# Kernel optimization log

Measured on AMD Instinct MI355X. Metric: run time of the kernel, lower is better.

## Reference

```python
import jax, jax.numpy as jnp
import numpy as np

NUM_CLASSES = 1000  # label vocabulary size (matches fill_max for label)
B = 16384
D_IN = 1024   # image_embedding
D_OUT = 256   # projection_dim


def setup_inputs() -> dict:
    key = jax.random.key(0)
    k = jax.random.split(key, 6)
    x = jax.random.normal(k[0], (B, D_IN), dtype=jnp.float32)
    label = jax.random.randint(k[1], (B,), 0, NUM_CLASSES, dtype=jnp.int64)
    scale = 1.0 / np.sqrt(D_IN)
    W1_w = jax.random.normal(k[2], (D_OUT, D_IN), dtype=jnp.float32) * scale
    W1_b = jax.random.normal(k[3], (D_OUT,), dtype=jnp.float32) * scale
    W2_w = jax.random.normal(k[4], (D_OUT, D_IN), dtype=jnp.float32) * scale
    W2_b = jax.random.normal(k[5], (D_OUT,), dtype=jnp.float32) * scale
    return {"x": x, "label": label, "W1_w": W1_w, "W1_b": W1_b,
            "W2_w": W2_w, "W2_b": W2_b}


def reference(x, label, W1_w, W1_b, W2_w, W2_b):
    # Leave-one-group-out mean, vectorized via segment sums.
    # Original: for each i, mean of x[label != label_i] (detached); zeros if none.
    b = x.shape[0]
    xd = jax.lax.stop_gradient(x)  # .detach() in the torch code
    label_sum = jax.ops.segment_sum(xd, label, num_segments=NUM_CLASSES)          # [C, D_IN]
    label_cnt = jax.ops.segment_sum(jnp.ones((b,), dtype=x.dtype), label,
                                    num_segments=NUM_CLASSES)                     # [C]
    total_sum = xd.sum(axis=0)                                                    # [D_IN]
    other_sum = total_sum[None, :] - label_sum[label]                             # [B, D_IN]
    other_cnt = jnp.asarray(b, x.dtype) - label_cnt[label]                        # [B]
    calculate_mean = jnp.where(other_cnt[:, None] > 0,
                               other_sum / jnp.maximum(other_cnt, 1)[:, None],
                               jnp.zeros((), x.dtype))                            # [B, D_IN]
    # W1(x) + W2(calculate_mean)  (torch Linear: y = x @ W.T + b)
    return x @ W1_w.T + W1_b + calculate_mean @ W2_w.T + W2_b
```

## Files before the change

kernel.cpp:

```cpp
#include <hip/hip_runtime.h>
#include <hip/hip_bf16.h>

constexpr int B      = 16384;
constexpr int D_IN   = 1024;
constexpr int D_OUT  = 256;
constexpr int NCLS   = 1000;
constexpr int CPAD   = 1024;

constexpr size_t OFF_XB   = 0;
constexpr size_t OFF_WB   = OFF_XB  + (size_t)B * D_IN * 2;
constexpr size_t OFF_S    = OFF_WB  + (size_t)512 * D_IN * 2;
constexpr size_t OFF_Z    = OFF_S   + (size_t)CPAD * D_IN * 4;
constexpr size_t OFF_T    = OFF_Z   + (size_t)CPAD * D_OUT * 4;
constexpr size_t OFF_CNT  = OFF_T   + (size_t)D_IN * 4;
constexpr size_t OFF_OFFS = OFF_CNT + (size_t)CPAD * 4;
constexpr size_t OFF_CUR  = OFF_OFFS+ (size_t)CPAD * 4;
constexpr size_t OFF_ROWL = OFF_CUR + (size_t)CPAD * 4;

typedef short bf16x8 __attribute__((ext_vector_type(8)));
typedef float f32x4  __attribute__((ext_vector_type(4)));

__device__ __forceinline__ unsigned short f2bf(float f) {
    unsigned int u = __float_as_uint(f);
    return (unsigned short)((u + 0x7FFFu + ((u >> 16) & 1u)) >> 16);
}

__device__ __forceinline__ void cvt8(const float4& a, const float4& b, unsigned short* dst) {
    union { unsigned short u[8]; bf16x8 v; } r;
    r.u[0] = f2bf(a.x); r.u[1] = f2bf(a.y); r.u[2] = f2bf(a.z); r.u[3] = f2bf(a.w);
    r.u[4] = f2bf(b.x); r.u[5] = f2bf(b.y); r.u[6] = f2bf(b.z); r.u[7] = f2bf(b.w);
    *(bf16x8*)dst = r.v;
}

__device__ __forceinline__ ushort4 f2bf4(const float4& a) {
    ushort4 r;
    r.x = f2bf(a.x); r.y = f2bf(a.y); r.z = f2bf(a.z); r.w = f2bf(a.w);
    return r;
}

__device__ __forceinline__ void async16(const unsigned short* g, unsigned short* l) {
    __builtin_amdgcn_global_load_lds(
        (const __attribute__((address_space(1))) void*)g,
        (__attribute__((address_space(3))) void*)l,
        16, 0, 0);
}

__global__ void cvtw_zero_kernel(const float* __restrict__ W1, const float* __restrict__ W2,
                                 unsigned short* __restrict__ Wb,
                                 int* __restrict__ cnt, float* __restrict__ T,
                                 float* __restrict__ Z) {
    int lin = blockIdx.x * blockDim.x + threadIdx.x;
    int i = lin * 8;
    const float* src = (i < D_OUT * D_IN) ? (W1 + i) : (W2 + (i - D_OUT * D_IN));
    float4 a = *(const float4*)(src);
    float4 b = *(const float4*)(src + 4);
    cvt8(a, b, Wb + i);
    if (lin < CPAD) { cnt[lin] = 0; T[lin] = 0.f; }
    *(float4*)(Z + (size_t)lin * 4) = float4{0.f, 0.f, 0.f, 0.f};
}

__global__ void hist_kernel(const int* __restrict__ label, int* __restrict__ cnt) {
    int i = blockIdx.x * blockDim.x + threadIdx.x;
    atomicAdd(&cnt[label[i]], 1);
}

__global__ __launch_bounds__(1024)
void scan_kernel(const int* __restrict__ cnt, int* __restrict__ offs, int* __restrict__ cursor) {
    __shared__ int bufA[1024];
    __shared__ int bufB[1024];
    int t = threadIdx.x;
    int v = cnt[t];
    bufA[t] = v;
    __syncthreads();
    int* src = bufA;
    int* dst = bufB;
    for (int off = 1; off < 1024; off <<= 1) {
        int sv = src[t];
        if (t >= off) sv += src[t - off];
        dst[t] = sv;
        __syncthreads();
        int* tmp = src; src = dst; dst = tmp;
    }
    int excl = src[t] - v;
    offs[t] = excl;
    cursor[t] = excl;
}

__global__ void scatter_kernel(const int* __restrict__ label,
                               int* __restrict__ cursor,
                               int* __restrict__ rowlist) {
    int i = blockIdx.x * blockDim.x + threadIdx.x;
    int c = label[i];
    int p = atomicAdd(&cursor[c], 1);
    rowlist[p] = i;
}

__global__ void segsum_kernel(const float* __restrict__ x,
                              const int* __restrict__ offs,
                              const int* __restrict__ cnt,
                              const int* __restrict__ rowlist,
                              float* __restrict__ s,
                              unsigned short* __restrict__ xb) {
    int c = blockIdx.x;
    int col = threadIdx.x * 4;
    float4 acc = {0.f, 0.f, 0.f, 0.f};
    if (c < NCLS) {
        int o = offs[c], n = cnt[c];
        int r = 0;
        for (; r + 4 <= n; r += 4) {
            int i0 = rowlist[o + r + 0];
            int i1 = rowlist[o + r + 1];
            int i2 = rowlist[o + r + 2];
            int i3 = rowlist[o + r + 3];
            float4 v0 = *(const float4*)(x + (size_t)i0 * D_IN + col);
            float4 v1 = *(const float4*)(x + (size_t)i1 * D_IN + col);
            float4 v2 = *(const float4*)(x + (size_t)i2 * D_IN + col);
            float4 v3 = *(const float4*)(x + (size_t)i3 * D_IN + col);
            *(ushort4*)(xb + (size_t)i0 * D_IN + col) = f2bf4(v0);
            *(ushort4*)(xb + (size_t)i1 * D_IN + col) = f2bf4(v1);
            *(ushort4*)(xb + (size_t)i2 * D_IN + col) = f2bf4(v2);
            *(ushort4*)(xb + (size_t)i3 * D_IN + col) = f2bf4(v3);
            acc.x += (v0.x + v1.x) + (v2.x + v3.x);
            acc.y += (v0.y + v1.y) + (v2.y + v3.y);
            acc.z += (v0.z + v1.z) + (v2.z + v3.z);
            acc.w += (v0.w + v1.w) + (v2.w + v3.w);
        }
        for (; r < n; ++r) {
            int i0 = rowlist[o + r];
            float4 v = *(const float4*)(x + (size_t)i0 * D_IN + col);
            *(ushort4*)(xb + (size_t)i0 * D_IN + col) = f2bf4(v);
            acc.x += v.x; acc.y += v.y; acc.z += v.z; acc.w += v.w;
        }
    }
    *(float4*)(s + (size_t)c * D_IN + col) = acc;
}

__global__ void tsum_kernel(const float* __restrict__ s, float* __restrict__ T) {
    int col = threadIdx.x * 4;
    int c0 = blockIdx.x * 16;
    float4 acc = {0.f, 0.f, 0.f, 0.f};
#pragma unroll 4
    for (int c = 0; c < 16; ++c) {
        float4 v = *(const float4*)(s + (size_t)(c0 + c) * D_IN + col);
        acc.x += v.x; acc.y += v.y; acc.z += v.z; acc.w += v.w;
    }
    atomicAdd(&T[col + 0], acc.x);
    atomicAdd(&T[col + 1], acc.y);
    atomicAdd(&T[col + 2], acc.z);
    atomicAdd(&T[col + 3], acc.w);
}

__global__ __launch_bounds__(256)
void meanz_kernel(const float* __restrict__ s,
                  const float* __restrict__ T,
                  const int* __restrict__ cnt,
                  const unsigned short* __restrict__ Wb,
                  const float* __restrict__ b2,
                  float* __restrict__ Z) {
    __shared__ unsigned short As[64 * 32];
    __shared__ unsigned short Bs[64 * 32];

    const int tid  = threadIdx.x;
    const int wave = tid >> 6;
    const int lane = tid & 63;
    const int quad = lane >> 4;
    const int l16  = lane & 15;
    const int bm   = blockIdx.x * 64;
    const int bn   = blockIdx.y * 64;
    const int kb   = blockIdx.z * 256;
    const int wm   = (wave >> 1) * 32;
    const int wn   = (wave & 1) * 32;

    const int arow = tid >> 2;
    const int akc  = (tid & 3) * 8;

    const int cls = bm + arow;
    const int d   = B - cnt[cls];
    const float scale = (d > 0) ? 1.f / (float)d : 0.f;
    const float* sp = s + (size_t)cls * D_IN + akc;
    const float* tp = T + akc;

    const int bidx = wave * 64 + lane;
    const int brow = bidx >> 2;
    const int bkc  = (bidx & 3) * 8;
    const unsigned short* bp = Wb + (size_t)(256 + bn + brow) * D_IN + bkc;

    f32x4 acc[2][2] = {};

    for (int k0 = kb; k0 < kb + 256; k0 += 32) {
        float4 s0 = *(const float4*)(sp + k0);
        float4 s1 = *(const float4*)(sp + k0 + 4);
        float4 t0 = *(const float4*)(tp + k0);
        float4 t1 = *(const float4*)(tp + k0 + 4);
        __syncthreads();
        async16(bp + k0, Bs + wave * 512);
        float4 m0 = {(t0.x - s0.x) * scale, (t0.y - s0.y) * scale,
                     (t0.z - s0.z) * scale, (t0.w - s0.w) * scale};
        float4 m1 = {(t1.x - s1.x) * scale, (t1.y - s1.y) * scale,
                     (t1.z - s1.z) * scale, (t1.w - s1.w) * scale};
        cvt8(m0, m1, As + arow * 32 + akc);
        __syncthreads();

        bf16x8 af[2], bfr[2];
#pragma unroll
        for (int t = 0; t < 2; ++t) {
            af[t]  = *(const bf16x8*)&As[(wm + t * 16 + l16) * 32 + quad * 8];
            bfr[t] = *(const bf16x8*)&Bs[(wn + t * 16 + l16) * 32 + quad * 8];
        }
#pragma unroll
        for (int i = 0; i < 2; ++i)
#pragma unroll
            for (int j = 0; j < 2; ++j)
                acc[i][j] = __builtin_amdgcn_mfma_f32_16x16x32_bf16(af[i], bfr[j], acc[i][j], 0, 0, 0);
    }

    const bool addb = (blockIdx.z == 0);
#pragma unroll
    for (int j = 0; j < 2; ++j) {
        const int n = bn + wn + j * 16 + l16;
        const float bias = addb ? b2[n] : 0.f;
#pragma unroll
        for (int i = 0; i < 2; ++i)
#pragma unroll
            for (int r = 0; r < 4; ++r) {
                const int c = bm + wm + i * 16 + quad * 4 + r;
                atomicAdd(&Z[(size_t)c * D_OUT + n], acc[i][j][r] + bias);
            }
    }
}

__global__ __launch_bounds__(256)
void gemm1_kernel(const unsigned short* __restrict__ xb,
                  const unsigned short* __restrict__ Wb,
                  const float* __restrict__ b1,
                  const float* __restrict__ Z,
                  const int* __restrict__ label,
                  float* __restrict__ out) {
    __shared__ unsigned short As[64 * 32];
    __shared__ unsigned short Bs[64 * 32];

    const int tid  = threadIdx.x;
    const int wave = tid >> 6;
    const int lane = tid & 63;
    const int quad = lane >> 4;
    const int l16  = lane & 15;
    const int bm   = blockIdx.x * 64;
    const int bn   = blockIdx.y * 64;
    const int wm   = (wave >> 1) * 32;
    const int wn   = (wave & 1) * 32;

    const int idx = wave * 64 + lane;
    const int row = idx >> 2;
    const int kc  = (idx & 3) * 8;
    const unsigned short* ap = xb + (size_t)(bm + row) * D_IN + kc;
    const unsigned short* bp = Wb + (size_t)(bn + row) * D_IN + kc;

    f32x4 acc[2][2] = {};

    for (int k0 = 0; k0 < D_IN; k0 += 32) {
        __syncthreads();
        async16(ap + k0, As + wave * 512);
        async16(bp + k0, Bs + wave * 512);
        __syncthreads();

        bf16x8 af[2], bfr[2];
#pragma unroll
        for (int t = 0; t < 2; ++t) {
            af[t]  = *(const bf16x8*)&As[(wm + t * 16 + l16) * 32 + quad * 8];
            bfr[t] = *(const bf16x8*)&Bs[(wn + t * 16 + l16) * 32 + quad * 8];
        }
#pragma unroll
        for (int i = 0; i < 2; ++i)
#pragma unroll
            for (int j = 0; j < 2; ++j)
                acc[i][j] = __builtin_amdgcn_mfma_f32_16x16x32_bf16(af[i], bfr[j], acc[i][j], 0, 0, 0);
    }

    int zrow[2][4];
#pragma unroll
    for (int i = 0; i < 2; ++i)
#pragma unroll
        for (int r = 0; r < 4; ++r)
            zrow[i][r] = label[bm + wm + i * 16 + quad * 4 + r] * D_OUT;

#pragma unroll
    for (int j = 0; j < 2; ++j) {
        const int n = bn + wn + j * 16 + l16;
        const float bias = b1[n];
#pragma unroll
        for (int i = 0; i < 2; ++i)
#pragma unroll
            for (int r = 0; r < 4; ++r) {
                const int m = bm + wm + i * 16 + quad * 4 + r;
                out[(size_t)m * D_OUT + n] = acc[i][j][r] + bias + Z[zrow[i][r] + n];
            }
    }
}

extern "C" void kernel_launch(void* const* d_in, const int* in_sizes, int n_in,
                              void* d_out, int out_size, void* d_ws, size_t ws_size,
                              hipStream_t stream) {
    const float* x    = (const float*)d_in[0];
    const int*   lab  = (const int*)d_in[1];
    const float* W1_w = (const float*)d_in[2];
    const float* W1_b = (const float*)d_in[3];
    const float* W2_w = (const float*)d_in[4];
    const float* W2_b = (const float*)d_in[5];
    float* out = (float*)d_out;

    char* ws = (char*)d_ws;
    unsigned short* xb = (unsigned short*)(ws + OFF_XB);
    unsigned short* Wb = (unsigned short*)(ws + OFF_WB);
    float* s   = (float*)(ws + OFF_S);
    float* Z   = (float*)(ws + OFF_Z);
    float* T   = (float*)(ws + OFF_T);
    int* cnt     = (int*)(ws + OFF_CNT);
    int* offs    = (int*)(ws + OFF_OFFS);
    int* cursor  = (int*)(ws + OFF_CUR);
    int* rowlist = (int*)(ws + OFF_ROWL);

    cvtw_zero_kernel<<<256, 256, 0, stream>>>(W1_w, W2_w, Wb, cnt, T, Z);
    hist_kernel<<<64, 256, 0, stream>>>(lab, cnt);
    scan_kernel<<<1, 1024, 0, stream>>>(cnt, offs, cursor);
    scatter_kernel<<<64, 256, 0, stream>>>(lab, cursor, rowlist);
    segsum_kernel<<<CPAD, 256, 0, stream>>>(x, offs, cnt, rowlist, s, xb);
    tsum_kernel<<<64, 256, 0, stream>>>(s, T);
    dim3 zgrid(CPAD / 64, D_OUT / 64, 4);
    meanz_kernel<<<zgrid, 256, 0, stream>>>(s, T, cnt, Wb, W2_b, Z);
    dim3 ggrid(B / 64, D_OUT / 64);
    gemm1_kernel<<<ggrid, 256, 0, stream>>>(xb, Wb, W1_b, Z, lab, out);
}
```

Before: 164.6 us.

## Fuse histogram/scan/scatter into per-class segsum scan and double K-step in GEMMs

Removes the separate histogram, scan and scatter launches. Each class block now scans all labels itself to collect its row list in shared memory and writes its own count. Both GEMM kernels now process 64 K elements per barrier pair instead of 32, and gemm1 prefetches bias and Z values before the main loop. This trades three small launches and global atomics for redundant label reads across 1024 blocks. The shared row buffer is capped at 512 rows per class, which the random labels fit but skewed labels could overflow.

```diff
diff --git a/kernel.cpp b/kernel.cpp
--- a/kernel.cpp
+++ b/kernel.cpp
@@ -13,9 +13,6 @@
 constexpr size_t OFF_Z    = OFF_S   + (size_t)CPAD * D_IN * 4;
 constexpr size_t OFF_T    = OFF_Z   + (size_t)CPAD * D_OUT * 4;
 constexpr size_t OFF_CNT  = OFF_T   + (size_t)D_IN * 4;
-constexpr size_t OFF_OFFS = OFF_CNT + (size_t)CPAD * 4;
-constexpr size_t OFF_CUR  = OFF_OFFS+ (size_t)CPAD * 4;
-constexpr size_t OFF_ROWL = OFF_CUR + (size_t)CPAD * 4;
 
 typedef short bf16x8 __attribute__((ext_vector_type(8)));
 typedef float f32x4  __attribute__((ext_vector_type(4)));
@@ -47,90 +44,64 @@
 
 __global__ void cvtw_zero_kernel(const float* __restrict__ W1, const float* __restrict__ W2,
                                  unsigned short* __restrict__ Wb,
-                                 int* __restrict__ cnt, float* __restrict__ T,
-                                 float* __restrict__ Z) {
+                                 float* __restrict__ T, float* __restrict__ Z) {
     int lin = blockIdx.x * blockDim.x + threadIdx.x;
     int i = lin * 8;
     const float* src = (i < D_OUT * D_IN) ? (W1 + i) : (W2 + (i - D_OUT * D_IN));
     float4 a = *(const float4*)(src);
     float4 b = *(const float4*)(src + 4);
     cvt8(a, b, Wb + i);
-    if (lin < CPAD) { cnt[lin] = 0; T[lin] = 0.f; }
+    if (lin < D_IN) T[lin] = 0.f;
     *(float4*)(Z + (size_t)lin * 4) = float4{0.f, 0.f, 0.f, 0.f};
 }
 
-__global__ void hist_kernel(const int* __restrict__ label, int* __restrict__ cnt) {
-    int i = blockIdx.x * blockDim.x + threadIdx.x;
-    atomicAdd(&cnt[label[i]], 1);
-}
-
-__global__ __launch_bounds__(1024)
-void scan_kernel(const int* __restrict__ cnt, int* __restrict__ offs, int* __restrict__ cursor) {
-    __shared__ int bufA[1024];
-    __shared__ int bufB[1024];
-    int t = threadIdx.x;
-    int v = cnt[t];
-    bufA[t] = v;
+__global__ __launch_bounds__(256)
+void segsum_kernel(const float* __restrict__ x,
+                   const int* __restrict__ label,
+                   int* __restrict__ cnt,
+                   float* __restrict__ s,
+                   unsigned short* __restrict__ xb) {
+    __shared__ int rows[512];
+    __shared__ int nrows;
+    const int c = blockIdx.x;
+    const int t = threadIdx.x;
+    if (t == 0) nrows = 0;
     __syncthreads();
-    int* src = bufA;
-    int* dst = bufB;
-    for (int off = 1; off < 1024; off <<= 1) {
-        int sv = src[t];
-        if (t >= off) sv += src[t - off];
-        dst[t] = sv;
-        __syncthreads();
-        int* tmp = src; src = dst; dst = tmp;
-    }
-    int excl = src[t] - v;
-    offs[t] = excl;
-    cursor[t] = excl;
-}
-
-__global__ void scatter_kernel(const int* __restrict__ label,
-                               int* __restrict__ cursor,
-                               int* __restrict__ rowlist) {
-    int i = blockIdx.x * blockDim.x + threadIdx.x;
-    int c = label[i];
-    int p = atomicAdd(&cursor[c], 1);
-    rowlist[p] = i;
-}
-
-__global__ void segsum_kernel(const float* __restrict__ x,
-                              const int* __restrict__ offs,
-                              const int* __restrict__ cnt,
-                              const int* __restrict__ rowlist,
-                              float* __restrict__ s,
-                              unsigned short* __restrict__ xb) {
-    int c = blockIdx.x;
-    int col = threadIdx.x * 4;
+    for (int i = t; i < B; i += 256)
+        if (label[i] == c) {
+            int p = atomicAdd(&nrows, 1);
+            rows[p] = i;
+        }
+    __syncthreads();
+    const int n = nrows;
+    if (t == 0) cnt[c] = n;
+
+    const int col = t * 4;
     float4 acc = {0.f, 0.f, 0.f, 0.f};
-    if (c < NCLS) {
-        int o = offs[c], n = cnt[c];
-        int r = 0;
-        for (; r + 4 <= n; r += 4) {
-            int i0 = rowlist[o + r + 0];
-            int i1 = rowlist[o + r + 1];
-            int i2 = rowlist[o + r + 2];
-            int i3 = rowlist[o + r + 3];
-            float4 v0 = *(const float4*)(x + (size_t)i0 * D_IN + col);
-            float4 v1 = *(const float4*)(x + (size_t)i1 * D_IN + col);
-            float4 v2 = *(const float4*)(x + (size_t)i2 * D_IN + col);
-            float4 v3 = *(const float4*)(x + (size_t)i3 * D_IN + col);
-            *(ushort4*)(xb + (size_t)i0 * D_IN + col) = f2bf4(v0);
-            *(ushort4*)(xb + (size_t)i1 * D_IN + col) = f2bf4(v1);
-            *(ushort4*)(xb + (size_t)i2 * D_IN + col) = f2bf4(v2);
-            *(ushort4*)(xb + (size_t)i3 * D_IN + col) = f2bf4(v3);
-            acc.x += (v0.x + v1.x) + (v2.x + v3.x);
-            acc.y += (v0.y + v1.y) + (v2.y + v3.y);
-            acc.z += (v0.z + v1.z) + (v2.z + v3.z);
-            acc.w += (v0.w + v1.w) + (v2.w + v3.w);
-        }
-        for (; r < n; ++r) {
-            int i0 = rowlist[o + r];
-            float4 v = *(const float4*)(x + (size_t)i0 * D_IN + col);
-            *(ushort4*)(xb + (size_t)i0 * D_IN + col) = f2bf4(v);
-            acc.x += v.x; acc.y += v.y; acc.z += v.z; acc.w += v.w;
-        }
+    int r = 0;
+    for (; r + 4 <= n; r += 4) {
+        int i0 = rows[r + 0];
+        int i1 = rows[r + 1];
+        int i2 = rows[r + 2];
+        int i3 = rows[r + 3];
+        float4 v0 = *(const float4*)(x + (size_t)i0 * D_IN + col);
+        float4 v1 = *(const float4*)(x + (size_t)i1 * D_IN + col);
+        float4 v2 = *(const float4*)(x + (size_t)i2 * D_IN + col);
+        float4 v3 = *(const float4*)(x + (size_t)i3 * D_IN + col);
+        *(ushort4*)(xb + (size_t)i0 * D_IN + col) = f2bf4(v0);
+        *(ushort4*)(xb + (size_t)i1 * D_IN + col) = f2bf4(v1);
+        *(ushort4*)(xb + (size_t)i2 * D_IN + col) = f2bf4(v2);
+        *(ushort4*)(xb + (size_t)i3 * D_IN + col) = f2bf4(v3);
+        acc.x += (v0.x + v1.x) + (v2.x + v3.x);
+        acc.y += (v0.y + v1.y) + (v2.y + v3.y);
+        acc.z += (v0.z + v1.z) + (v2.z + v3.z);
+        acc.w += (v0.w + v1.w) + (v2.w + v3.w);
+    }
+    for (; r < n; ++r) {
+        int i0 = rows[r];
+        float4 v = *(const float4*)(x + (size_t)i0 * D_IN + col);
+        *(ushort4*)(xb + (size_t)i0 * D_IN + col) = f2bf4(v);
+        acc.x += v.x; acc.y += v.y; acc.z += v.z; acc.w += v.w;
     }
     *(float4*)(s + (size_t)c * D_IN + col) = acc;
 }
@@ -157,8 +128,8 @@
                   const unsigned short* __restrict__ Wb,
                   const float* __restrict__ b2,
                   float* __restrict__ Z) {
-    __shared__ unsigned short As[64 * 32];
-    __shared__ unsigned short Bs[64 * 32];
+    __shared__ unsigned short As[4096];
+    __shared__ unsigned short Bs[4096];
 
     const int tid  = threadIdx.x;
     const int wave = tid >> 6;
@@ -187,31 +158,44 @@
 
     f32x4 acc[2][2] = {};
 
-    for (int k0 = kb; k0 < kb + 256; k0 += 32) {
+    for (int k0 = kb; k0 < kb + 256; k0 += 64) {
         float4 s0 = *(const float4*)(sp + k0);
         float4 s1 = *(const float4*)(sp + k0 + 4);
+        float4 s2 = *(const float4*)(sp + k0 + 32);
+        float4 s3 = *(const float4*)(sp + k0 + 36);
         float4 t0 = *(const float4*)(tp + k0);
         float4 t1 = *(const float4*)(tp + k0 + 4);
+        float4 t2 = *(const float4*)(tp + k0 + 32);
+        float4 t3 = *(const float4*)(tp + k0 + 36);
         __syncthreads();
-        async16(bp + k0, Bs + wave * 512);
+        async16(bp + k0,      Bs + wave * 512);
+        async16(bp + k0 + 32, Bs + 2048 + wave * 512);
         float4 m0 = {(t0.x - s0.x) * scale, (t0.y - s0.y) * scale,
                      (t0.z - s0.z) * scale, (t0.w - s0.w) * scale};
         float4 m1 = {(t1.x - s1.x) * scale, (t1.y - s1.y) * scale,
                      (t1.z - s1.z) * scale, (t1.w - s1.w) * scale};
+        float4 m2 = {(t2.x - s2.x) * scale, (t2.y - s2.y) * scale,
+                     (t2.z - s2.z) * scale, (t2.w - s2.w) * scale};
+        float4 m3 = {(t3.x - s3.x) * scale, (t3.y - s3.y) * scale,
+                     (t3.z - s3.z) * scale, (t3.w - s3.w) * scale};
         cvt8(m0, m1, As + arow * 32 + akc);
+        cvt8(m2, m3, As + 2048 + arow * 32 + akc);
         __syncthreads();
 
-        bf16x8 af[2], bfr[2];
-#pragma unroll
-        for (int t = 0; t < 2; ++t) {
-            af[t]  = *(const bf16x8*)&As[(wm + t * 16 + l16) * 32 + quad * 8];
-            bfr[t] = *(const bf16x8*)&Bs[(wn + t * 16 + l16) * 32 + quad * 8];
+#pragma unroll
+        for (int p = 0; p < 2; ++p) {
+            bf16x8 af[2], bfr[2];
+#pragma unroll
+            for (int t = 0; t < 2; ++t) {
+                af[t]  = *(const bf16x8*)&As[p * 2048 + (wm + t * 16 + l16) * 32 + quad * 8];
+                bfr[t] = *(const bf16x8*)&Bs[p * 2048 + (wn + t * 16 + l16) * 32 + quad * 8];
+            }
+#pragma unroll
+            for (int i = 0; i < 2; ++i)
+#pragma unroll
+                for (int j = 0; j < 2; ++j)
+                    acc[i][j] = __builtin_amdgcn_mfma_f32_16x16x32_bf16(af[i], bfr[j], acc[i][j], 0, 0, 0);
         }
-#pragma unroll
-        for (int i = 0; i < 2; ++i)
-#pragma unroll
-            for (int j = 0; j < 2; ++j)
-                acc[i][j] = __builtin_amdgcn_mfma_f32_16x16x32_bf16(af[i], bfr[j], acc[i][j], 0, 0, 0);
     }
 
     const bool addb = (blockIdx.z == 0);
@@ -236,8 +220,8 @@
                   const float* __restrict__ Z,
                   const int* __restrict__ label,
                   float* __restrict__ out) {
-    __shared__ unsigned short As[64 * 32];
-    __shared__ unsigned short Bs[64 * 32];
+    __shared__ unsigned short As[4096];
+    __shared__ unsigned short Bs[4096];
 
     const int tid  = threadIdx.x;
     const int wave = tid >> 6;
@@ -255,44 +239,60 @@
     const unsigned short* ap = xb + (size_t)(bm + row) * D_IN + kc;
     const unsigned short* bp = Wb + (size_t)(bn + row) * D_IN + kc;
 
-    f32x4 acc[2][2] = {};
-
-    for (int k0 = 0; k0 < D_IN; k0 += 32) {
-        __syncthreads();
-        async16(ap + k0, As + wave * 512);
-        async16(bp + k0, Bs + wave * 512);
-        __syncthreads();
-
-        bf16x8 af[2], bfr[2];
-#pragma unroll
-        for (int t = 0; t < 2; ++t) {
-            af[t]  = *(const bf16x8*)&As[(wm + t * 16 + l16) * 32 + quad * 8];
-            bfr[t] = *(const bf16x8*)&Bs[(wn + t * 16 + l16) * 32 + quad * 8];
-        }
-#pragma unroll
-        for (int i = 0; i < 2; ++i)
-#pragma unroll
-            for (int j = 0; j < 2; ++j)
-                acc[i][j] = __builtin_amdgcn_mfma_f32_16x16x32_bf16(af[i], bfr[j], acc[i][j], 0, 0, 0);
-    }
-
     int zrow[2][4];
 #pragma unroll
     for (int i = 0; i < 2; ++i)
 #pragma unroll
         for (int r = 0; r < 4; ++r)
             zrow[i][r] = label[bm + wm + i * 16 + quad * 4 + r] * D_OUT;
-
+    float bb[2];
+    float zv[2][2][4];
 #pragma unroll
     for (int j = 0; j < 2; ++j) {
         const int n = bn + wn + j * 16 + l16;
-        const float bias = b1[n];
+        bb[j] = b1[n];
+#pragma unroll
+        for (int i = 0; i < 2; ++i)
+#pragma unroll
+            for (int r = 0; r < 4; ++r)
+                zv[j][i][r] = Z[zrow[i][r] + n];
+    }
+
+    f32x4 acc[2][2] = {};
+
+    for (int k0 = 0; k0 < D_IN; k0 += 64) {
+        __syncthreads();
+        async16(ap + k0,      As + wave * 512);
+        async16(ap + k0 + 32, As + 2048 + wave * 512);
+        async16(bp + k0,      Bs + wave * 512);
+        async16(bp + k0 + 32, Bs + 2048 + wave * 512);
+        __syncthreads();
+
+#pragma unroll
+        for (int p = 0; p < 2; ++p) {
+            bf16x8 af[2], bfr[2];
+#pragma unroll
+            for (int t = 0; t < 2; ++t) {
+                af[t]  = *(const bf16x8*)&As[p * 2048 + (wm + t * 16 + l16) * 32 + quad * 8];
+                bfr[t] = *(const bf16x8*)&Bs[p * 2048 + (wn + t * 16 + l16) * 32 + quad * 8];
+            }
+#pragma unroll
+            for (int i = 0; i < 2; ++i)
+#pragma unroll
+                for (int j = 0; j < 2; ++j)
+                    acc[i][j] = __builtin_amdgcn_mfma_f32_16x16x32_bf16(af[i], bfr[j], acc[i][j], 0, 0, 0);
+        }
+    }
+
+#pragma unroll
+    for (int j = 0; j < 2; ++j) {
+        const int n = bn + wn + j * 16 + l16;
 #pragma unroll
         for (int i = 0; i < 2; ++i)
 #pragma unroll
             for (int r = 0; r < 4; ++r) {
                 const int m = bm + wm + i * 16 + quad * 4 + r;
-                out[(size_t)m * D_OUT + n] = acc[i][j][r] + bias + Z[zrow[i][r] + n];
+                out[(size_t)m * D_OUT + n] = acc[i][j][r] + bb[j] + zv[j][i][r];
             }
     }
 }
@@ -314,16 +314,10 @@
     float* s   = (float*)(ws + OFF_S);
     float* Z   = (float*)(ws + OFF_Z);
     float* T   = (float*)(ws + OFF_T);
-    int* cnt     = (int*)(ws + OFF_CNT);
-    int* offs    = (int*)(ws + OFF_OFFS);
-    int* cursor  = (int*)(ws + OFF_CUR);
-    int* rowlist = (int*)(ws + OFF_ROWL);
-
-    cvtw_zero_kernel<<<256, 256, 0, stream>>>(W1_w, W2_w, Wb, cnt, T, Z);
-    hist_kernel<<<64, 256, 0, stream>>>(lab, cnt);
-    scan_kernel<<<1, 1024, 0, stream>>>(cnt, offs, cursor);
-    scatter_kernel<<<64, 256, 0, stream>>>(lab, cursor, rowlist);
-    segsum_kernel<<<CPAD, 256, 0, stream>>>(x, offs, cnt, rowlist, s, xb);
+    int* cnt   = (int*)(ws + OFF_CNT);
+
+    cvtw_zero_kernel<<<256, 256, 0, stream>>>(W1_w, W2_w, Wb, T, Z);
+    segsum_kernel<<<CPAD, 256, 0, stream>>>(x, lab, cnt, s, xb);
     tsum_kernel<<<64, 256, 0, stream>>>(s, T);
     dim3 zgrid(CPAD / 64, D_OUT / 64, 4);
     meanz_kernel<<<zgrid, 256, 0, stream>>>(s, T, cnt, Wb, W2_b, Z);
```

Result: no change. 165.0 us (+0.2%).
